# Kernel tuning notes

Hardware: AMD Instinct MI355X
Metric: run time of the kernel (lower is better)

## Reference

```python
import jax, jax.numpy as jnp
import numpy as np

B, N, M, R = 128, 511, 256, 64
IN = 512  # word_dim + tag_dim


def setup_inputs() -> dict:
    key = jax.random.key(0)
    ks = jax.random.split(key, 16)
    def w(k, shape, fan_in):
        return jax.random.normal(k, shape, dtype=jnp.float32) / np.sqrt(fan_in)
    inp = {
        "word_tag_emb": jax.random.normal(ks[0], (B, N, IN), dtype=jnp.float32),
        "rel_emb": jax.random.normal(ks[1], (B, N, R), dtype=jnp.float32),
        "n_nodes": N,
    }
    for j, nm in enumerate(["ix", "fx", "ux", "ox"]):
        inp["W" + nm] = w(ks[2 + j], (IN, M), IN)
        inp["b" + nm] = jnp.zeros((M,), jnp.float32)
    for j, nm in enumerate(["ih", "fh", "uh", "oh"]):
        inp["W" + nm] = w(ks[6 + j], (M, M), M)
        inp["b" + nm] = jnp.zeros((M,), jnp.float32)
    # seq_lstm (nn.LSTM, 1 layer): gate order i, f, g, o; stored [in, 4M]
    inp["W_seq_ih"] = w(ks[10], (M + R, 4 * M), M + R)
    inp["W_seq_hh"] = w(ks[11], (M, 4 * M), M)
    inp["b_seq_ih"] = jnp.zeros((4 * M,), jnp.float32)
    inp["b_seq_hh"] = jnp.zeros((4 * M,), jnp.float32)
    return inp


def reference(word_tag_emb, rel_emb,
              Wix, bix, Wfx, bfx, Wux, bux, Wox, box,
              Wih, bih, Wfh, bfh, Wuh, buh, Woh, boh,
              W_seq_ih, W_seq_hh, b_seq_ih, b_seq_hh, n_nodes):
    Bn, Nn, _ = word_tag_emb.shape
    Mm = Wih.shape[0]
    dt = word_tag_emb.dtype

    def lstm_cell(x, h, c):
        g = x @ W_seq_ih + h @ W_seq_hh + (b_seq_ih + b_seq_hh)
        i, f, gg, o = jnp.split(g, 4, axis=-1)
        c2 = jax.nn.sigmoid(f) * c + jax.nn.sigmoid(i) * jnp.tanh(gg)
        return jax.nn.sigmoid(o) * jnp.tanh(c2), c2

    def step(carry, node):
        h_buf, c_buf = carry  # [B, N, M] state buffers
        ch = jnp.stack([2 * node + 1, 2 * node + 2])        # heap children
        valid = (ch < Nn).astype(dt)[:, None, None]          # [2,1,1]
        idx = jnp.minimum(ch, Nn - 1)
        ch_h = jnp.take(h_buf, idx, axis=1).transpose(1, 0, 2) * valid   # [2,B,M]
        ch_c = jnp.take(c_buf, idx, axis=1).transpose(1, 0, 2) * valid   # [2,B,M]
        ch_r = jnp.take(rel_emb, idx, axis=1).transpose(1, 0, 2) * valid # [2,B,R]
        # seq_lstm over the (masked) child sequence: input [h_j ; rel_j]
        hs = jnp.zeros((Bn, Mm), dt)
        cs = jnp.zeros((Bn, Mm), dt)
        for j in range(2):  # fixed max_children (binary tree)
            hn, cn = lstm_cell(jnp.concatenate([ch_h[j], ch_r[j]], -1), hs, cs)
            hs = valid[j] * hn + (1.0 - valid[j]) * hs
            cs = valid[j] * cn + (1.0 - valid[j]) * cs
        h_tilde = hs  # stays zero at leaves (seq_lstm never run there)
        x = word_tag_emb[:, node]  # [B, IN]
        i = jax.nn.sigmoid(x @ Wix + bix + h_tilde @ Wih + bih)
        o = jax.nn.sigmoid(x @ Wox + box + h_tilde @ Woh + boh)
        u = jnp.tanh(x @ Wux + bux + h_tilde @ Wuh + buh)
        f = jax.nn.sigmoid((x @ Wfx + bfx)[None] + ch_h @ Wfh + bfh)  # [2,B,M]
        c = i * u + jnp.sum(f * ch_c * valid, axis=0)
        h = o * jnp.tanh(c)
        h_buf = h_buf.at[:, node].set(h)
        c_buf = c_buf.at[:, node].set(c)
        return (h_buf, c_buf), None

    h0 = jnp.zeros((Bn, Nn, Mm), dt)
    c0 = jnp.zeros((Bn, Nn, Mm), dt)
    nodes = jnp.arange(Nn - 1, -1, -1)  # bottom-up (children before parents)
    (h_buf, c_buf), _ = jax.lax.scan(step, (h0, c0), nodes)
    return h_buf[:, 0]  # root hidden state, [B, M]
```

## Files before the change

kernel.cpp:

```cpp
#include <hip/hip_runtime.h>
#include <math.h>

#define NNODE 511

typedef short s16x8 __attribute__((ext_vector_type(8)));
typedef float f32x4 __attribute__((ext_vector_type(4)));

__device__ __forceinline__ unsigned short f2bf(float f) {
  unsigned int u = __builtin_bit_cast(unsigned int, f);
  u += 0x7fffu + ((u >> 16) & 1u);
  return (unsigned short)(u >> 16);
}
__device__ __forceinline__ float sigf(float x) {
  float e = __builtin_amdgcn_exp2f(-1.442695040888963f * x);
  return __builtin_amdgcn_rcpf(1.0f + e);
}
__device__ __forceinline__ float tanh_a(float x) {
  float e = __builtin_amdgcn_exp2f(2.885390081777927f * x);
  return 1.0f - 2.0f * __builtin_amdgcn_rcpf(1.0f + e);
}

__device__ __forceinline__ void load16_lds(const unsigned short* g, unsigned short* l) {
  __builtin_amdgcn_global_load_lds(
      (const __attribute__((address_space(1))) void*)g,
      (__attribute__((address_space(3))) void*)l, 16, 0, 0);
}

__device__ __forceinline__ void swz_blk(int& bx, int& by) {
  bx = blockIdx.x; by = blockIdx.y;
  int ny = gridDim.y;
  if ((ny & 7) == 0) {
    int lin = by * 8 + bx;
    int w = lin >> 3;
    by = (lin & 7) * (ny >> 3) + (w >> 3);
    bx = w & 7;
  }
}

__global__ void k_prep_x(const float* __restrict__ w, unsigned short* __restrict__ xbf) {
  int o = (blockIdx.x * 256 + threadIdx.x) * 4;
  int node = o >> 16;
  int b = (o >> 9) & 127;
  int k = o & 511;
  const float4 v = *(const float4*)(w + ((size_t)b * NNODE + node) * 512 + k);
  unsigned int p0 = (unsigned int)f2bf(v.x) | ((unsigned int)f2bf(v.y) << 16);
  unsigned int p1 = (unsigned int)f2bf(v.z) | ((unsigned int)f2bf(v.w) << 16);
  *(uint2*)(xbf + o) = make_uint2(p0, p1);
}

__global__ void k_prep_w(const float* __restrict__ Wix, const float* __restrict__ Wux,
                         const float* __restrict__ Wox, const float* __restrict__ Wfx,
                         const float* __restrict__ Wih, const float* __restrict__ Wuh,
                         const float* __restrict__ Woh, const float* __restrict__ Wfh,
                         const float* __restrict__ Wsi, const float* __restrict__ Wsh,
                         unsigned short* __restrict__ WL2t, unsigned short* __restrict__ WA2t,
                         unsigned short* __restrict__ WH2t, unsigned short* __restrict__ WEX2t) {
  int idx = blockIdx.x * 256 + threadIdx.x;
  if (idx < 393216) {
    int c = idx >> 9, k = idx & 511;
    int G = c / 48, rem = c - G * 48, g = rem >> 4, mi = rem & 15, m = G * 16 + mi;
    const float* W = (g == 0) ? Wix : (g == 1) ? Wux : Wox;
    WL2t[idx] = f2bf(W[k * 256 + m]);
  } else if (idx < 802816) {
    int o = idx - 393216;
    int c = o / 320, k = o - c * 320;
    int G = c / 80, rem = c - G * 80, g = rem >> 4, mi = rem & 15, m = G * 16 + mi;
    float v;
    if (g < 4) v = Wsi[k * 1024 + g * 256 + m];
    else       v = (k < 256) ? Wfh[k * 256 + m] : 0.0f;
    WA2t[o] = f2bf(v);
  } else if (idx < 1064960) {
    int o = idx - 802816;
    int c = o >> 8, k = o & 255;
    int G = c >> 6, rem = c & 63, g = rem >> 4, mi = rem & 15, m = G * 16 + mi;
    WH2t[o] = f2bf(Wsh[k * 1024 + g * 256 + m]);
  } else if (idx < 1851392) {
    int o = idx - 1064960;
    int c = o / 768, k = o - c * 768;
    int G = c >> 6, rem = c & 63, g = rem >> 4, mi = rem & 15, m = G * 16 + mi;
    float v;
    if (k < 256) {
      v = (g == 0) ? Wih[k * 256 + m] : (g == 1) ? Wuh[k * 256 + m]
        : (g == 2) ? Woh[k * 256 + m] : 0.0f;
    } else {
      int k2 = k - 256;
      v = (g == 0) ? Wix[k2 * 256 + m] : (g == 1) ? Wux[k2 * 256 + m]
        : (g == 2) ? Wox[k2 * 256 + m] : Wfx[k2 * 256 + m];
    }
    WEX2t[o] = f2bf(v);
  }
}

#define MFMA_BODY(NG, CW)                                                     \
  _Pragma("unroll")                                                           \
  for (int kk = 0; kk < 64; kk += 32) {                                       \
    const int sw = (kk | (q * 8)) ^ ((m16 & 7) * 8);                          \
    s16x8 af[4], bfr[NG];                                                     \
    _Pragma("unroll")                                                         \
    for (int i = 0; i < 4; ++i)                                               \
      af[i] = *(const s16x8*)(&As[(wm + i * 16 + m16) * 64 + sw]);            \
    _Pragma("unroll")                                                         \
    for (int j = 0; j < NG; ++j)                                              \
      bfr[j] = *(const s16x8*)(&Bs[(wc * CW + j * 16 + m16) * 64 + sw]);      \
    _Pragma("unroll")                                                         \
    for (int i = 0; i < 4; ++i)                                               \
      _Pragma("unroll")                                                       \
      for (int j = 0; j < NG; ++j)                                            \
        acc[i][j] = __builtin_amdgcn_mfma_f32_16x16x32_bf16(af[i], bfr[j], acc[i][j], 0, 0, 0); \
  }

#define STAGE(DST, SRC, STRIDE, R)                                            \
  _Pragma("unroll")                                                           \
  for (int c = 0; c < (R) / 32; ++c) {                                        \
    int row8 = wave * ((R) / 4) + c * 8;                                      \
    load16_lds(SRC + (size_t)(row8 + l8) * (STRIDE) + k0 + gsw, &DST[row8 * 64]); \
  }

__global__ __launch_bounds__(256) void k_gemm1(
    const unsigned short* __restrict__ AinL, const unsigned short* __restrict__ AinR,
    const unsigned short* __restrict__ Bt,
    unsigned short* __restrict__ h1, float* __restrict__ c1,
    float* __restrict__ FHL, float* __restrict__ FHR, float* __restrict__ PR,
    const float* __restrict__ bsi, const float* __restrict__ bsh, int crows) {
  __shared__ alignas(16) unsigned short As[128 * 64];
  __shared__ alignas(16) unsigned short Bs[160 * 64];
  int bx, by; swz_blk(bx, by);
  const int t = threadIdx.x;
  const int wave = t >> 6, lane = t & 63;
  const int wm = (wave & 1) * 64, wc = wave >> 1;
  const int m16 = lane & 15, q = lane >> 4;
  const int l8 = lane >> 3, l7 = lane & 7;
  const int gsw = ((l7 ^ l8) * 8);
  const int rowBase = by * 128;
  const bool isL = rowBase < crows;
  const unsigned short* Arow = isL ? (AinL + (size_t)rowBase * 320)
                                   : (AinR + (size_t)(rowBase - crows) * 320);
  const unsigned short* Brow = Bt + (size_t)bx * 160 * 320;
  f32x4 acc[4][5] = {};

  for (int k0 = 0; k0 < 320; k0 += 64) {
    STAGE(As, Arow, 320, 128)
    STAGE(Bs, Brow, 320, 160)
    __syncthreads();
    MFMA_BODY(5, 80)
    __syncthreads();
  }

  const int m = (bx * 2 + wc) * 16 + m16;
  if (isL) {
    float bi = bsi[m] + bsh[m];
    float bg = bsi[512 + m] + bsh[512 + m];
    float bo = bsi[768 + m] + bsh[768 + m];
#pragma unroll
    for (int i = 0; i < 4; ++i)
#pragma unroll
      for (int r2 = 0; r2 < 4; ++r2) {
        int r = rowBase + wm + i * 16 + q * 4 + r2;
        float ii = sigf(acc[i][0][r2] + bi);
        float gg = tanh_a(acc[i][2][r2] + bg);
        float oo = sigf(acc[i][3][r2] + bo);
        float cv = ii * gg;
        size_t o = (size_t)r * 256 + m;
        h1[o] = f2bf(oo * tanh_a(cv));
        c1[o] = cv;
        FHL[o] = acc[i][4][r2];
      }
  } else {
#pragma unroll
    for (int i = 0; i < 4; ++i)
#pragma unroll
      for (int r2 = 0; r2 < 4; ++r2) {
        int rr = rowBase - crows + wm + i * 16 + q * 4 + r2;
        size_t o = (size_t)rr * 256 + m;
        float4 pv = {acc[i][0][r2], acc[i][1][r2], acc[i][2][r2], acc[i][3][r2]};
        *(float4*)(PR + o * 4) = pv;
        FHR[o] = acc[i][4][r2];
      }
  }
}

__global__ __launch_bounds__(256) void k_gemm2(
    const unsigned short* __restrict__ A, const unsigned short* __restrict__ Bt,
    const float* __restrict__ PR, const float* __restrict__ c1,
    unsigned short* __restrict__ HT,
    const float* __restrict__ bsi, const float* __restrict__ bsh) {
  __shared__ alignas(16) unsigned short As[128 * 64];
  __shared__ alignas(16) unsigned short Bs[128 * 64];
  int bx, by; swz_blk(bx, by);
  const int t = threadIdx.x;
  const int wave = t >> 6, lane = t & 63;
  const int wm = (wave & 1) * 64, wc = wave >> 1;
  const int m16 = lane & 15, q = lane >> 4;
  const int l8 = lane >> 3, l7 = lane & 7;
  const int gsw = ((l7 ^ l8) * 8);
  const int rowBase = by * 128;
  const unsigned short* Arow = A + (size_t)rowBase * 256;
  const unsigned short* Brow = Bt + (size_t)bx * 128 * 256;
  f32x4 acc[4][4] = {};

  for (int k0 = 0; k0 < 256; k0 += 64) {
    STAGE(As, Arow, 256, 128)
    STAGE(Bs, Brow, 256, 128)
    __syncthreads();
    MFMA_BODY(4, 64)
    __syncthreads();
  }

  const int m = (bx * 2 + wc) * 16 + m16;
  float b0 = bsi[m] + bsh[m];
  float b1 = bsi[256 + m] + bsh[256 + m];
  float b2 = bsi[512 + m] + bsh[512 + m];
  float b3 = bsi[768 + m] + bsh[768 + m];
#pragma unroll
  for (int i = 0; i < 4; ++i)
#pragma unroll
    for (int r2 = 0; r2 < 4; ++r2) {
      int r = rowBase + wm + i * 16 + q * 4 + r2;
      size_t o = (size_t)r * 256 + m;
      float4 pv = *(const float4*)(PR + o * 4);
      float ii = sigf(acc[i][0][r2] + pv.x + b0);
      float ff = sigf(acc[i][1][r2] + pv.y + b1);
      float gg = tanh_a(acc[i][2][r2] + pv.z + b2);
      float oo = sigf(acc[i][3][r2] + pv.w + b3);
      float c2 = ff * c1[o] + ii * gg;
      HT[o] = f2bf(oo * tanh_a(c2));
    }
}

__global__ __launch_bounds__(256) void k_gemm3(
    const unsigned short* __restrict__ HT, const unsigned short* __restrict__ xnode,
    const unsigned short* __restrict__ Bt,
    const float* __restrict__ FHL, const float* __restrict__ FHR,
    float* __restrict__ cbuf, unsigned short* __restrict__ Ain,
    const float* __restrict__ rel, float* __restrict__ out,
    const float* __restrict__ bix, const float* __restrict__ bih,
    const float* __restrict__ bux, const float* __restrict__ buh,
    const float* __restrict__ box, const float* __restrict__ boh,
    const float* __restrict__ bfx, const float* __restrict__ bfh,
    int base, int v0, int n, int lvl) {
  __shared__ alignas(16) unsigned short As[128 * 64];
  __shared__ alignas(16) unsigned short Bs[128 * 64];
  int bx, by; swz_blk(bx, by);
  const int t = threadIdx.x;
  const int wave = t >> 6, lane = t & 63;
  const int wm = (wave & 1) * 64, wc = wave >> 1;
  const int m16 = lane & 15, q = lane >> 4;
  const int l8 = lane >> 3, l7 = lane & 7;
  const int gsw = ((l7 ^ l8) * 8);
  const int rowBase = by * 128;
  const unsigned short* Brow = Bt + (size_t)bx * 128 * 768;
  f32x4 acc[4][4] = {};

  for (int kb = 0; kb < 768; kb += 64) {
    {
      const unsigned short* Arow;
      int k0;
      if (kb < 256) { Arow = HT + (size_t)rowBase * 256;    k0 = kb; 
#pragma unroll
        for (int c = 0; c < 4; ++c) {
          int row8 = wave * 32 + c * 8;
          load16_lds(Arow + (size_t)(row8 + l8) * 256 + k0 + gsw, &As[row8 * 64]);
        }
      } else {        Arow = xnode + (size_t)rowBase * 512; k0 = kb - 256;
#pragma unroll
        for (int c = 0; c < 4; ++c) {
          int row8 = wave * 32 + c * 8;
          load16_lds(Arow + (size_t)(row8 + l8) * 512 + k0 + gsw, &As[row8 * 64]);
        }
      }
    }
    {
      int k0 = kb;
      STAGE(Bs, Brow, 768, 128)
    }
    __syncthreads();
    MFMA_BODY(4, 64)
    __syncthreads();
  }

  const int m = (bx * 2 + wc) * 16 + m16;
  float bi = bix[m] + bih[m];
  float bu = bux[m] + buh[m];
  float bo = box[m] + boh[m];
  float bf = bfx[m] + bfh[m];
#pragma unroll
  for (int i = 0; i < 4; ++i)
#pragma unroll
    for (int r2 = 0; r2 < 4; ++r2) {
      int r = rowBase + wm + i * 16 + q * 4 + r2;
      int vloc = r >> 7, b = r & 127;
      int vg = v0 + vloc;
      int node = base + vg;
      int ch0 = 2 * node + 1;
      size_t o = (size_t)r * 256 + m;
      float pf = acc[i][3][r2] + bf;
      float f0 = sigf(pf + FHL[o]);
      float f1 = sigf(pf + FHR[o]);
      float ii = sigf(acc[i][0][r2] + bi);
      float uu = tanh_a(acc[i][1][r2] + bu);
      float oo = sigf(acc[i][2][r2] + bo);
      float cc = ii * uu + f0 * cbuf[((size_t)ch0 * 128 + b) * 256 + m]
                         + f1 * cbuf[((size_t)(ch0 + 1) * 128 + b) * 256 + m];
      float hh = oo * tanh_a(cc);
      if (lvl == 0) {
        out[b * 256 + m] = hh;
      } else {
        cbuf[((size_t)node * 128 + b) * 256 + m] = cc;
        int rowA = (vg & 1) * (n >> 1) * 128 + (vg >> 1) * 128 + b;
        Ain[(size_t)rowA * 320 + m] = f2bf(hh);
        if (m < 64)
          Ain[(size_t)rowA * 320 + 256 + m] = f2bf(rel[((size_t)b * NNODE + node) * 64 + m]);
      }
    }
}

__global__ __launch_bounds__(256) void k_leaf(
    const unsigned short* __restrict__ xleaf, const unsigned short* __restrict__ Bt,
    float* __restrict__ cbuf, unsigned short* __restrict__ Ain,
    const float* __restrict__ rel,
    const float* __restrict__ bix, const float* __restrict__ bih,
    const float* __restrict__ bux, const float* __restrict__ buh,
    const float* __restrict__ box, const float* __restrict__ boh) {
  __shared__ alignas(16) unsigned short As[128 * 64];
  __shared__ alignas(16) unsigned short Bs[96 * 64];
  int bx, by; swz_blk(bx, by);
  const int t = threadIdx.x;
  const int wave = t >> 6, lane = t & 63;
  const int wm = (wave & 1) * 64, wc = wave >> 1;
  const int m16 = lane & 15, q = lane >> 4;
  const int l8 = lane >> 3, l7 = lane & 7;
  const int gsw = ((l7 ^ l8) * 8);
  const int rowBase = by * 128;
  const unsigned short* Arow = xleaf + (size_t)rowBase * 512;
  const unsigned short* Brow = Bt + (size_t)bx * 96 * 512;
  f32x4 acc[4][3] = {};

  for (int k0 = 0; k0 < 512; k0 += 64) {
    STAGE(As, Arow, 512, 128)
#pragma unroll
    for (int c = 0; c < 3; ++c) {
      int row8 = wave * 24 + c * 8;
      load16_lds(Brow + (size_t)(row8 + l8) * 512 + k0 + gsw, &Bs[row8 * 64]);
    }
    __syncthreads();
    MFMA_BODY(3, 48)
    __syncthreads();
  }

  const int m = (bx * 2 + wc) * 16 + m16;
  float bi = bix[m] + bih[m];
  float bu = bux[m] + buh[m];
  float bo = box[m] + boh[m];
#pragma unroll
  for (int i = 0; i < 4; ++i)
#pragma unroll
    for (int r2 = 0; r2 < 4; ++r2) {
      int r = rowBase + wm + i * 16 + q * 4 + r2;
      int vg = r >> 7, b = r & 127;
      int node = 255 + vg;
      float ii = sigf(acc[i][0][r2] + bi);
      float uu = tanh_a(acc[i][1][r2] + bu);
      float oo = sigf(acc[i][2][r2] + bo);
      float cc = ii * uu;
      float hh = oo * tanh_a(cc);
      cbuf[((size_t)node * 128 + b) * 256 + m] = cc;
      int rowA = (vg & 1) * 16384 + (vg >> 1) * 128 + b;
      Ain[(size_t)rowA * 320 + m] = f2bf(hh);
      if (m < 64)
        Ain[(size_t)rowA * 320 + 256 + m] = f2bf(rel[((size_t)b * NNODE + node) * 64 + m]);
    }
}

extern "C" void kernel_launch(void* const* d_in, const int* in_sizes, int n_in,
                              void* d_out, int out_size, void* d_ws, size_t ws_size,
                              hipStream_t stream) {
  const float* wte = (const float*)d_in[0];
  const float* rel = (const float*)d_in[1];
  const float* Wix = (const float*)d_in[3];
  const float* bix = (const float*)d_in[4];
  const float* Wfx = (const float*)d_in[5];
  const float* bfx = (const float*)d_in[6];
  const float* Wux = (const float*)d_in[7];
  const float* bux = (const float*)d_in[8];
  const float* Wox = (const float*)d_in[9];
  const float* box = (const float*)d_in[10];
  const float* Wih = (const float*)d_in[11];
  const float* bih = (const float*)d_in[12];
  const float* Wfh = (const float*)d_in[13];
  const float* bfh = (const float*)d_in[14];
  const float* Wuh = (const float*)d_in[15];
  const float* buh = (const float*)d_in[16];
  const float* Woh = (const float*)d_in[17];
  const float* boh = (const float*)d_in[18];
  const float* Wsi = (const float*)d_in[19];
  const float* Wsh = (const float*)d_in[20];
  const float* bsi = (const float*)d_in[21];
  const float* bsh = (const float*)d_in[22];
  float* out = (float*)d_out;
  (void)in_sizes; (void)n_in; (void)out_size;

  int INT_MAXN;
  if (ws_size >= (size_t)310 * 1024 * 1024)      INT_MAXN = 128;
  else if (ws_size >= (size_t)200 * 1024 * 1024) INT_MAXN = 32;
  else                                           INT_MAXN = 8;
  const int crowsMax = INT_MAXN * 128;

  char* ws = (char*)d_ws;
  size_t off = 0;
  auto alloc = [&](size_t bytes) {
    size_t o = off; off += (bytes + 255) & ~(size_t)255; return o;
  };
  unsigned short* xbf  = (unsigned short*)(ws + alloc((size_t)NNODE * 128 * 512 * 2));
  float*          cbuf = (float*)         (ws + alloc((size_t)NNODE * 128 * 256 * 4));
  unsigned short* Ain  = (unsigned short*)(ws + alloc((size_t)32768 * 320 * 2));
  unsigned short* WL2t = (unsigned short*)(ws + alloc((size_t)768 * 512 * 2));
  unsigned short* WA2t = (unsigned short*)(ws + alloc((size_t)1280 * 320 * 2));
  unsigned short* WH2t = (unsigned short*)(ws + alloc((size_t)1024 * 256 * 2));
  unsigned short* WEX2t= (unsigned short*)(ws + alloc((size_t)1024 * 768 * 2));
  unsigned short* h1   = (unsigned short*)(ws + alloc((size_t)crowsMax * 256 * 2));
  float*          c1   = (float*)         (ws + alloc((size_t)crowsMax * 256 * 4));
  float*          FHL  = (float*)         (ws + alloc((size_t)crowsMax * 256 * 4));
  float*          FHR  = (float*)         (ws + alloc((size_t)crowsMax * 256 * 4));
  float*          PR   = (float*)         (ws + alloc((size_t)crowsMax * 1024 * 4));
  unsigned short* HT   = (unsigned short*)(ws + alloc((size_t)crowsMax * 256 * 2));

  k_prep_x<<<32704, 256, 0, stream>>>(wte, xbf);
  k_prep_w<<<7232, 256, 0, stream>>>(Wix, Wux, Wox, Wfx, Wih, Wuh, Woh, Wfh,
                                     Wsi, Wsh, WL2t, WA2t, WH2t, WEX2t);

  k_leaf<<<dim3(8, 256), 256, 0, stream>>>(xbf + (size_t)255 * 128 * 512, WL2t,
                                           cbuf, Ain, rel, bix, bih, bux, buh, box, boh);

  for (int lvl = 7; lvl >= 0; --lvl) {
    int n = 1 << lvl;
    int base = n - 1;
    int cn = (n < INT_MAXN) ? n : INT_MAXN;
    for (int v0 = 0; v0 < n; v0 += cn) {
      int crows = cn * 128;
      const unsigned short* AinL = Ain + (size_t)(v0 * 128) * 320;
      const unsigned short* AinR = Ain + (size_t)((n + v0) * 128) * 320;
      const unsigned short* xnode = xbf + (size_t)(base + v0) * 128 * 512;
      k_gemm1<<<dim3(8, 2 * cn), 256, 0, stream>>>(AinL, AinR, WA2t, h1, c1,
                                                   FHL, FHR, PR, bsi, bsh, crows);
      k_gemm2<<<dim3(8, cn), 256, 0, stream>>>(h1, WH2t, PR, c1, HT, bsi, bsh);
      k_gemm3<<<dim3(8, cn), 256, 0, stream>>>(HT, xnode, WEX2t, FHL, FHR, cbuf, Ain,
                                               rel, out, bix, bih, bux, buh, box, boh,
                                               bfx, bfh, base, v0, n, lvl);
    }
  }
}
```

Before: 883.4 us.

## Double-buffer LDS tiles in all GEMM kernels to overlap loads with MFMA

Each GEMM kernel (gemm1, gemm2, gemm3, leaf) now keeps two LDS buffers for A and B. It issues the global-to-LDS loads for the next K tile before running the MFMA work on the current tile, with a sched_barrier that keeps the compiler from reordering the two. The aim is to hide global load latency behind matrix math and remove one barrier per iteration. The cost is twice the LDS per block, which can lower occupancy. Correctness relies on the __syncthreads at the end of each iteration, since global_load_lds completion is not waited on explicitly before the next read.

```diff
diff --git a/kernel.cpp b/kernel.cpp
--- a/kernel.cpp
+++ b/kernel.cpp
@@ -91,17 +91,17 @@
   }
 }
 
-#define MFMA_BODY(NG, CW)                                                     \
+#define MFMA_BODY(AP, BP, NG, CW)                                             \
   _Pragma("unroll")                                                           \
   for (int kk = 0; kk < 64; kk += 32) {                                       \
     const int sw = (kk | (q * 8)) ^ ((m16 & 7) * 8);                          \
     s16x8 af[4], bfr[NG];                                                     \
     _Pragma("unroll")                                                         \
     for (int i = 0; i < 4; ++i)                                               \
-      af[i] = *(const s16x8*)(&As[(wm + i * 16 + m16) * 64 + sw]);            \
+      af[i] = *(const s16x8*)(&(AP)[(wm + i * 16 + m16) * 64 + sw]);          \
     _Pragma("unroll")                                                         \
     for (int j = 0; j < NG; ++j)                                              \
-      bfr[j] = *(const s16x8*)(&Bs[(wc * CW + j * 16 + m16) * 64 + sw]);      \
+      bfr[j] = *(const s16x8*)(&(BP)[(wc * CW + j * 16 + m16) * 64 + sw]);    \
     _Pragma("unroll")                                                         \
     for (int i = 0; i < 4; ++i)                                               \
       _Pragma("unroll")                                                       \
@@ -109,11 +109,11 @@
         acc[i][j] = __builtin_amdgcn_mfma_f32_16x16x32_bf16(af[i], bfr[j], acc[i][j], 0, 0, 0); \
   }
 
-#define STAGE(DST, SRC, STRIDE, R)                                            \
+#define STAGE(DST, SRC, STRIDE, R, K0)                                        \
   _Pragma("unroll")                                                           \
   for (int c = 0; c < (R) / 32; ++c) {                                        \
     int row8 = wave * ((R) / 4) + c * 8;                                      \
-    load16_lds(SRC + (size_t)(row8 + l8) * (STRIDE) + k0 + gsw, &DST[row8 * 64]); \
+    load16_lds(SRC + (size_t)(row8 + l8) * (STRIDE) + (K0) + gsw, &(DST)[row8 * 64]); \
   }
 
 __global__ __launch_bounds__(256) void k_gemm1(
@@ -122,8 +122,8 @@
     unsigned short* __restrict__ h1, float* __restrict__ c1,
     float* __restrict__ FHL, float* __restrict__ FHR, float* __restrict__ PR,
     const float* __restrict__ bsi, const float* __restrict__ bsh, int crows) {
-  __shared__ alignas(16) unsigned short As[128 * 64];
-  __shared__ alignas(16) unsigned short Bs[160 * 64];
+  __shared__ alignas(16) unsigned short As[2][128 * 64];
+  __shared__ alignas(16) unsigned short Bs[2][160 * 64];
   int bx, by; swz_blk(bx, by);
   const int t = threadIdx.x;
   const int wave = t >> 6, lane = t & 63;
@@ -138,11 +138,17 @@
   const unsigned short* Brow = Bt + (size_t)bx * 160 * 320;
   f32x4 acc[4][5] = {};
 
-  for (int k0 = 0; k0 < 320; k0 += 64) {
-    STAGE(As, Arow, 320, 128)
-    STAGE(Bs, Brow, 320, 160)
-    __syncthreads();
-    MFMA_BODY(5, 80)
+  STAGE(As[0], Arow, 320, 128, 0)
+  STAGE(Bs[0], Brow, 320, 160, 0)
+  __syncthreads();
+#pragma unroll
+  for (int ti = 0; ti < 5; ++ti) {
+    if (ti < 4) {
+      STAGE(As[(ti + 1) & 1], Arow, 320, 128, (ti + 1) * 64)
+      STAGE(Bs[(ti + 1) & 1], Brow, 320, 160, (ti + 1) * 64)
+    }
+    __builtin_amdgcn_sched_barrier(0);
+    MFMA_BODY(As[ti & 1], Bs[ti & 1], 5, 80)
     __syncthreads();
   }
 
@@ -184,8 +190,8 @@
     const float* __restrict__ PR, const float* __restrict__ c1,
     unsigned short* __restrict__ HT,
     const float* __restrict__ bsi, const float* __restrict__ bsh) {
-  __shared__ alignas(16) unsigned short As[128 * 64];
-  __shared__ alignas(16) unsigned short Bs[128 * 64];
+  __shared__ alignas(16) unsigned short As[2][128 * 64];
+  __shared__ alignas(16) unsigned short Bs[2][128 * 64];
   int bx, by; swz_blk(bx, by);
   const int t = threadIdx.x;
   const int wave = t >> 6, lane = t & 63;
@@ -198,11 +204,17 @@
   const unsigned short* Brow = Bt + (size_t)bx * 128 * 256;
   f32x4 acc[4][4] = {};
 
-  for (int k0 = 0; k0 < 256; k0 += 64) {
-    STAGE(As, Arow, 256, 128)
-    STAGE(Bs, Brow, 256, 128)
-    __syncthreads();
-    MFMA_BODY(4, 64)
+  STAGE(As[0], Arow, 256, 128, 0)
+  STAGE(Bs[0], Brow, 256, 128, 0)
+  __syncthreads();
+#pragma unroll
+  for (int ti = 0; ti < 4; ++ti) {
+    if (ti < 3) {
+      STAGE(As[(ti + 1) & 1], Arow, 256, 128, (ti + 1) * 64)
+      STAGE(Bs[(ti + 1) & 1], Brow, 256, 128, (ti + 1) * 64)
+    }
+    __builtin_amdgcn_sched_barrier(0);
+    MFMA_BODY(As[ti & 1], Bs[ti & 1], 4, 64)
     __syncthreads();
   }
 
@@ -238,8 +250,8 @@
     const float* __restrict__ box, const float* __restrict__ boh,
     const float* __restrict__ bfx, const float* __restrict__ bfh,
     int base, int v0, int n, int lvl) {
-  __shared__ alignas(16) unsigned short As[128 * 64];
-  __shared__ alignas(16) unsigned short Bs[128 * 64];
+  __shared__ alignas(16) unsigned short As[2][128 * 64];
+  __shared__ alignas(16) unsigned short Bs[2][128 * 64];
   int bx, by; swz_blk(bx, by);
   const int t = threadIdx.x;
   const int wave = t >> 6, lane = t & 63;
@@ -251,30 +263,36 @@
   const unsigned short* Brow = Bt + (size_t)bx * 128 * 768;
   f32x4 acc[4][4] = {};
 
-  for (int kb = 0; kb < 768; kb += 64) {
-    {
-      const unsigned short* Arow;
-      int k0;
-      if (kb < 256) { Arow = HT + (size_t)rowBase * 256;    k0 = kb; 
-#pragma unroll
-        for (int c = 0; c < 4; ++c) {
-          int row8 = wave * 32 + c * 8;
-          load16_lds(Arow + (size_t)(row8 + l8) * 256 + k0 + gsw, &As[row8 * 64]);
-        }
-      } else {        Arow = xnode + (size_t)rowBase * 512; k0 = kb - 256;
-#pragma unroll
-        for (int c = 0; c < 4; ++c) {
-          int row8 = wave * 32 + c * 8;
-          load16_lds(Arow + (size_t)(row8 + l8) * 512 + k0 + gsw, &As[row8 * 64]);
-        }
-      }
-    }
-    {
-      int k0 = kb;
-      STAGE(Bs, Brow, 768, 128)
-    }
-    __syncthreads();
-    MFMA_BODY(4, 64)
+  auto stageA = [&](unsigned short* dst, int kb) {
+    if (kb < 256) {
+      const unsigned short* Arow = HT + (size_t)rowBase * 256;
+#pragma unroll
+      for (int c = 0; c < 4; ++c) {
+        int row8 = wave * 32 + c * 8;
+        load16_lds(Arow + (size_t)(row8 + l8) * 256 + kb + gsw, &dst[row8 * 64]);
+      }
+    } else {
+      const unsigned short* Arow = xnode + (size_t)rowBase * 512;
+      int k0 = kb - 256;
+#pragma unroll
+      for (int c = 0; c < 4; ++c) {
+        int row8 = wave * 32 + c * 8;
+        load16_lds(Arow + (size_t)(row8 + l8) * 512 + k0 + gsw, &dst[row8 * 64]);
+      }
+    }
+  };
+
+  stageA(As[0], 0);
+  STAGE(Bs[0], Brow, 768, 128, 0)
+  __syncthreads();
+#pragma unroll
+  for (int ti = 0; ti < 12; ++ti) {
+    if (ti < 11) {
+      stageA(As[(ti + 1) & 1], (ti + 1) * 64);
+      STAGE(Bs[(ti + 1) & 1], Brow, 768, 128, (ti + 1) * 64)
+    }
+    __builtin_amdgcn_sched_barrier(0);
+    MFMA_BODY(As[ti & 1], Bs[ti & 1], 4, 64)
     __syncthreads();
   }
 
@@ -321,8 +339,8 @@
     const float* __restrict__ bix, const float* __restrict__ bih,
     const float* __restrict__ bux, const float* __restrict__ buh,
     const float* __restrict__ box, const float* __restrict__ boh) {
-  __shared__ alignas(16) unsigned short As[128 * 64];
-  __shared__ alignas(16) unsigned short Bs[96 * 64];
+  __shared__ alignas(16) unsigned short As[2][128 * 64];
+  __shared__ alignas(16) unsigned short Bs[2][96 * 64];
   int bx, by; swz_blk(bx, by);
   const int t = threadIdx.x;
   const int wave = t >> 6, lane = t & 63;
@@ -335,15 +353,26 @@
   const unsigned short* Brow = Bt + (size_t)bx * 96 * 512;
   f32x4 acc[4][3] = {};
 
-  for (int k0 = 0; k0 < 512; k0 += 64) {
-    STAGE(As, Arow, 512, 128)
-#pragma unroll
-    for (int c = 0; c < 3; ++c) {
-      int row8 = wave * 24 + c * 8;
-      load16_lds(Brow + (size_t)(row8 + l8) * 512 + k0 + gsw, &Bs[row8 * 64]);
-    }
-    __syncthreads();
-    MFMA_BODY(3, 48)
+  STAGE(As[0], Arow, 512, 128, 0)
+#pragma unroll
+  for (int c = 0; c < 3; ++c) {
+    int row8 = wave * 24 + c * 8;
+    load16_lds(Brow + (size_t)(row8 + l8) * 512 + 0 + gsw, &Bs[0][row8 * 64]);
+  }
+  __syncthreads();
+#pragma unroll
+  for (int ti = 0; ti < 8; ++ti) {
+    if (ti < 7) {
+      int kn = (ti + 1) * 64;
+      STAGE(As[(ti + 1) & 1], Arow, 512, 128, kn)
+#pragma unroll
+      for (int c = 0; c < 3; ++c) {
+        int row8 = wave * 24 + c * 8;
+        load16_lds(Brow + (size_t)(row8 + l8) * 512 + kn + gsw, &Bs[(ti + 1) & 1][row8 * 64]);
+      }
+    }
+    __builtin_amdgcn_sched_barrier(0);
+    MFMA_BODY(As[ti & 1], Bs[ti & 1], 3, 48)
     __syncthreads();
   }
 
```

Result: faster. 788.7 us (-10.7%).
